# Optimization experiments

Hardware: AMD Instinct MI355X
Metric: run time of the kernel (lower is better)

## Reference

```python
import jax, jax.numpy as jnp
import numpy as np

H, W, NUM_HEADS = 32, 32, 8


def dwconv3x3(x, w, b):
    # x: (B,C,H,W), w: (C,1,3,3) depthwise, b: (C,)
    y = jax.lax.conv_general_dilated(
        x, w, window_strides=(1, 1), padding='SAME',
        dimension_numbers=('NCHW', 'OIHW', 'NCHW'),
        feature_group_count=x.shape[1])
    return y + b[None, :, None, None]


def conv1x1(x, w, b):
    # x: (B,C,H,W), w: (O,C), b: (O,)
    return jnp.einsum('oc,bchw->bohw', w, x) + b[None, :, None, None]


def layernorm(x, w, b, eps=1e-6):
    mu = x.mean(-1, keepdims=True)
    var = ((x - mu) ** 2).mean(-1, keepdims=True)
    return (x - mu) / jnp.sqrt(var + eps) * w + b


def setup_inputs() -> dict:
    key = jax.random.key(0)
    ks = jax.random.split(key, 12)
    B, N, C = 32, H * W, 512
    Ch = 4 * C  # inverted MLP hidden
    s_lin = 0.02
    s_dw = np.sqrt(2.0 / 9.0)   # fan_out init for 3x3 depthwise
    s_pw1 = np.sqrt(2.0 / Ch)
    s_pw2 = np.sqrt(2.0 / C)
    return {
        'x': jax.random.normal(ks[0], (B, N, C), jnp.float32),
        'cpe_w': jax.random.normal(ks[1], (C, 1, 3, 3), jnp.float32) * s_dw,
        'cpe_b': jnp.zeros((C,), jnp.float32),
        'ln1_w': jnp.ones((C,), jnp.float32),
        'ln1_b': jnp.zeros((C,), jnp.float32),
        'qkv_w': jax.random.normal(ks[2], (3 * C, C), jnp.float32) * s_lin,
        'crpe_w': jax.random.normal(ks[3], (C, 1, 3, 3), jnp.float32) * s_dw,
        'crpe_b': jnp.zeros((C,), jnp.float32),
        'ln2_w': jnp.ones((C,), jnp.float32),
        'ln2_b': jnp.zeros((C,), jnp.float32),
        'fc1_w': jax.random.normal(ks[4], (Ch, C), jnp.float32) * s_pw1,
        'fc1_b': jnp.zeros((Ch,), jnp.float32),
        'dw_w': jax.random.normal(ks[5], (Ch, 1, 3, 3), jnp.float32) * s_dw,
        'dw_b': jnp.zeros((Ch,), jnp.float32),
        'fc2_w': jax.random.normal(ks[6], (C, Ch), jnp.float32) * s_pw2,
        'fc2_b': jnp.zeros((C,), jnp.float32),
    }


def reference(x, cpe_w, cpe_b, ln1_w, ln1_b, qkv_w, crpe_w, crpe_b,
              ln2_w, ln2_b, fc1_w, fc1_b, dw_w, dw_b, fc2_w, fc2_b):
    B, N, C = x.shape
    h = NUM_HEADS
    d = C // h
    scale = d ** -0.5

    # --- Convolutional position encoding: x = x + dwconv(x) ---
    img = x.reshape(B, H, W, C).transpose(0, 3, 1, 2)  # B C H W
    img = img + dwconv3x3(img, cpe_w, cpe_b)
    x = img.transpose(0, 2, 3, 1).reshape(B, N, C)

    # --- Factorized attention + conv relative position encoding ---
    cur = layernorm(x, ln1_w, ln1_b)
    qkv = cur @ qkv_w.T                                 # (B,N,3C)
    qkv = qkv.reshape(B, N, 3, h, d).transpose(2, 0, 3, 1, 4)  # (3,B,h,N,d)
    q, k, v = qkv[0], qkv[1], qkv[2]
    k_softmax = jax.nn.softmax(k, axis=2)               # softmax over tokens N
    ktv = jnp.einsum('bhnk,bhnv->bhkv', k_softmax, v)   # (B,h,d,d)
    factor_att = jnp.einsum('bhnk,bhkv->bhnv', q, ktv)  # (B,h,N,d)
    # crpe: depthwise conv on v as image, elementwise-multiplied by q
    v_img = v.transpose(0, 1, 3, 2).reshape(B, h * d, H, W)
    v_img = dwconv3x3(v_img, crpe_w, crpe_b)
    v_conv = v_img.reshape(B, h, d, N).transpose(0, 1, 3, 2)
    crpe = q * v_conv
    attn_out = (scale * factor_att + crpe).transpose(0, 2, 1, 3).reshape(B, N, C)
    x = x + attn_out

    # --- Inverted MLP (conv-based channel mixing) ---
    cur = layernorm(x, ln2_w, ln2_b)
    img = cur.reshape(B, H, W, C).transpose(0, 3, 1, 2)  # B C H W
    hdn = conv1x1(img, fc1_w, fc1_b)
    hdn = jax.nn.gelu(hdn, approximate=False)
    hdn = hdn + dwconv3x3(hdn, dw_w, dw_b)
    out = conv1x1(hdn, fc2_w, fc2_b)
    x = x + out.transpose(0, 2, 3, 1).reshape(B, N, C)
    return x
```

## Files before the change

kernel.cpp:

```cpp
#include <hip/hip_runtime.h>
#include <hip/hip_bf16.h>

using bf16 = __hip_bfloat16;
using s16x4 = __attribute__((ext_vector_type(4))) short;
using s16x8 = __attribute__((ext_vector_type(8))) short;
using f32x4 = __attribute__((ext_vector_type(4))) float;

#define DI __device__ __forceinline__

template <int N> DI void wvm() {
    if constexpr (N == 8) asm volatile("s_waitcnt vmcnt(8)" ::: "memory");
    else if constexpr (N == 4) asm volatile("s_waitcnt vmcnt(4)" ::: "memory");
    else if constexpr (N == 2) asm volatile("s_waitcnt vmcnt(2)" ::: "memory");
    else asm volatile("s_waitcnt vmcnt(0)" ::: "memory");
}

DI float b2f(short s) { union { unsigned u; float f; } z; z.u = ((unsigned)(unsigned short)s) << 16; return z.f; }
DI short f2b(float f) { bf16 t = __float2bfloat16(f); return *(short*)&t; }

DI float gelu_f(float x) {
    const float t = 0.7978845608f * x * (1.f + 0.044715f * x * x);
    const float e = __expf(2.f * t);
    const float th = 1.f - 2.f / (e + 1.f);
    return 0.5f * x * (1.f + th);
}

DI void ld8(const bf16* p, float* f) {
    s16x8 x = *(const s16x8*)(const void*)p;
#pragma unroll
    for (int c = 0; c < 8; c++) f[c] = b2f(x[c]);
}
DI void ld8(const float* p, float* f) {
    float4 a = *(const float4*)p, b = *(const float4*)(p + 4);
    f[0]=a.x; f[1]=a.y; f[2]=a.z; f[3]=a.w; f[4]=b.x; f[5]=b.y; f[6]=b.z; f[7]=b.w;
}

typedef const __attribute__((address_space(1))) void* gp_t;
typedef __attribute__((address_space(3))) void* lp_t;
DI void gload_lds16(const void* g, void* l) {
    __builtin_amdgcn_global_load_lds((gp_t)g, (lp_t)l, 16, 0, 0);
}

__global__ void diag_k(float* out, float v) { out[0] = v; }

__global__ void f2bf_k(const float* __restrict__ in, bf16* __restrict__ out, int n) {
    int i = (blockIdx.x * 256 + threadIdx.x) * 8;
    if (i >= n) return;
    float f[8];
    ld8(in + i, f);
    s16x8 o;
#pragma unroll
    for (int c = 0; c < 8; c++) o[c] = f2b(f[c]);
    *(s16x8*)(void*)(out + i) = o;
}

__global__ void f2bf_w2_k(const float* __restrict__ in, bf16* __restrict__ out) {
    const int i = (blockIdx.x * 256 + threadIdx.x) * 8;
    const int n = i >> 11, c = i & 2047;
    const int h = c >> 10, k = c & 1023;
    float f[8];
    ld8(in + i, f);
    s16x8 o;
#pragma unroll
    for (int e = 0; e < 8; e++) o[e] = f2b(f[e]);
    *(s16x8*)(void*)(out + (size_t)h * 524288 + n * 1024 + k) = o;
}

DI void tap10(const float* r, float w0, float w1, float w2, float* acc) {
#pragma unroll
    for (int i = 0; i < 8; i++)
        acc[i] += w0 * r[i] + w1 * r[i + 1] + w2 * r[i + 2];
}

template <typename TI, typename TO, bool RESID, int CPL>
__global__ __launch_bounds__(256) void conv4_k(
    const TI* in, long rs, long coff,
    const float* __restrict__ w, const float* __restrict__ bias,
    TO* out, long ors, int gshift)
{
    constexpr int CH = 64 * CPL;
    constexpr int ECNT = CH / 8;
    __shared__ float buf[2][CH][33];
    const int t = threadIdx.x;
    const int band = blockIdx.x & 3;
    const int cg = (blockIdx.x >> 2) & ((1 << gshift) - 1);
    const int img = blockIdx.x >> (2 + gshift);
    const int y0 = band * 8;

    const int spx = t >> 3;
    const int sce = (t & 7) * ECNT;
    const TI* gsrc = in + ((long)img << 10) * rs + coff + (long)cg * CH + sce;

    const int c = t & 63;
    const int xb = (t >> 6) * 8;

    float wv9[9][CPL], bw[CPL];
#pragma unroll
    for (int p = 0; p < CPL; p++) {
        const int gch = cg * CH + c * CPL + p;
#pragma unroll
        for (int j = 0; j < 9; j++) wv9[j][p] = w[gch * 9 + j];
        bw[p] = bias[gch];
    }

    auto stage = [&](int row) {
        float f[ECNT];
        ld8(gsrc + (long)(row * 32 + spx) * rs, f);
        if constexpr (ECNT == 16) ld8(gsrc + (long)(row * 32 + spx) * rs + 8, f + 8);
        float* d = &buf[row & 1][0][0];
#pragma unroll
        for (int k = 0; k < ECNT; k++) {
            const int ch = sce + k;
            const int rr = (CPL == 2) ? ((ch & 1) * 64 + (ch >> 1)) : ch;
            d[rr * 33 + spx] = f[k];
        }
    };
    auto slice = [&](int row, float r[CPL][10]) {
#pragma unroll
        for (int p = 0; p < CPL; p++) {
            const float* s = &buf[row & 1][c + p * 64][0];
            r[p][0] = (xb == 0) ? 0.f : s[xb - 1];
#pragma unroll
            for (int i = 0; i < 8; i++) r[p][1 + i] = s[xb + i];
            r[p][9] = (xb + 8 >= 32) ? 0.f : s[xb + 8];
        }
    };
    auto zero = [&](float r[CPL][10]) {
#pragma unroll
        for (int p = 0; p < CPL; p++)
#pragma unroll
            for (int i = 0; i < 10; i++) r[p][i] = 0.f;
    };

    float r0[CPL][10], r1[CPL][10], r2[CPL][10];
    if (y0 > 0) stage(y0 - 1);
    __syncthreads();
    if (y0 > 0) slice(y0 - 1, r0); else zero(r0);
    stage(y0);
    __syncthreads();
    slice(y0, r1);

    for (int y = y0; y < y0 + 8; ++y) {
        const int yn = y + 1;
        if (yn <= 31) stage(yn);
        __syncthreads();
        if (yn <= 31) slice(yn, r2); else zero(r2);
        float acc[CPL][8];
#pragma unroll
        for (int p = 0; p < CPL; p++) {
#pragma unroll
            for (int i = 0; i < 8; i++) acc[p][i] = bw[p];
            tap10(r0[p], wv9[0][p], wv9[1][p], wv9[2][p], acc[p]);
            tap10(r1[p], wv9[3][p], wv9[4][p], wv9[5][p], acc[p]);
            tap10(r2[p], wv9[6][p], wv9[7][p], wv9[8][p], acc[p]);
            if (RESID) {
#pragma unroll
                for (int i = 0; i < 8; i++) acc[p][i] += r1[p][i + 1];
            }
        }
        TO* o = out + ((long)(img * 1024 + y * 32 + xb)) * ors + (long)cg * CH + c * CPL;
#pragma unroll
        for (int i = 0; i < 8; i++) {
            if constexpr (CPL == 2 && sizeof(TO) == 2) {
                const unsigned u = (unsigned)(unsigned short)f2b(acc[0][i]) |
                                   ((unsigned)(unsigned short)f2b(acc[1][i]) << 16);
                *(unsigned*)(void*)(o + (long)i * ors) = u;
            } else {
                o[(long)i * ors] = (TO)acc[0][i];
            }
        }
#pragma unroll
        for (int p = 0; p < CPL; p++)
#pragma unroll
            for (int i = 0; i < 10; i++) { r0[p][i] = r1[p][i]; r1[p][i] = r2[p][i]; }
    }
}

__global__ __launch_bounds__(256) void ln_k(const float* __restrict__ x,
                                            const float* __restrict__ w,
                                            const float* __restrict__ bp,
                                            bf16* __restrict__ out)
{
    const size_t row = blockIdx.x * 4 + (threadIdx.x >> 6);
    const int t = threadIdx.x & 63;
    const float* xr = x + row * 512;
    alignas(16) float v[8];
    *(float4*)&v[0] = *(const float4*)(xr + t * 8);
    *(float4*)&v[4] = *(const float4*)(xr + t * 8 + 4);
    float s = 0.f;
#pragma unroll
    for (int j = 0; j < 8; j++) s += v[j];
#pragma unroll
    for (int mm = 32; mm; mm >>= 1) s += __shfl_xor(s, mm);
    const float mu = s * (1.f / 512.f);
    float q = 0.f;
#pragma unroll
    for (int j = 0; j < 8; j++) { v[j] -= mu; q += v[j] * v[j]; }
#pragma unroll
    for (int mm = 32; mm; mm >>= 1) q += __shfl_xor(q, mm);
    const float rstd = rsqrtf(q * (1.f / 512.f) + 1e-6f);
    alignas(16) float wv[8], bv[8];
    *(float4*)&wv[0] = *(const float4*)(w + t * 8);
    *(float4*)&wv[4] = *(const float4*)(w + t * 8 + 4);
    *(float4*)&bv[0] = *(const float4*)(bp + t * 8);
    *(float4*)&bv[4] = *(const float4*)(bp + t * 8 + 4);
    alignas(16) bf16 o[8];
#pragma unroll
    for (int j = 0; j < 8; j++) o[j] = __float2bfloat16(v[j] * rstd * wv[j] + bv[j]);
    *(uint4*)(out + row * 512 + t * 8) = *(const uint4*)o;
}

template <int EPI, int K>
__global__ __launch_bounds__(512) void gemm8p_k(
    const bf16* __restrict__ A, const bf16* __restrict__ Bw,
    const float* __restrict__ bias, const float* resid,
    bf16* __restrict__ outb, float* outf, int M, int Nn)
{
    constexpr int KT = K / 64;
    __shared__ __align__(16) char lds[131072];
    char* ldsA = lds;
    char* ldsB = lds + 65536;
    const int t = threadIdx.x;
    const int lane = t & 63;
    const int w = t >> 6;
    const int wr = w >> 2, wc = w & 3;
    const int m0 = blockIdx.x * 256;
    const int n0 = blockIdx.y * 256;
    const int lr = lane & 15, lg = lane >> 4;

    f32x4 acc[8][4] = {};

    const int srow = lane >> 3;
    const int ssrc = 8 * ((lane & 7) ^ srow);

    auto SA = [&](int b, int kt, int h) {
#pragma unroll
        for (int j = 0; j < 2; j++) {
            const int lrow0 = j * 64 + w * 8;
            const int R0 = j * 128 + h * 64 + (lrow0 & 63);
            gload_lds16(A + (size_t)(m0 + R0 + srow) * K + kt * 64 + ssrc,
                        ldsA + ((b * 2 + h) * 128 + lrow0) * 128);
        }
    };
    auto SB = [&](int b, int kt, int h) {
#pragma unroll
        for (int j = 0; j < 2; j++) {
            const int lrow0 = j * 64 + w * 8;
            const int R0 = (lrow0 >> 5) * 64 + h * 32 + (lrow0 & 31);
            gload_lds16(Bw + (size_t)(n0 + R0 + srow) * K + kt * 64 + ssrc,
                        ldsB + ((b * 2 + h) * 128 + lrow0) * 128);
        }
    };
    auto RA = [&](int b, int h, int m, int ks) -> s16x8 {
        return *(const s16x8*)(ldsA + ((b * 2 + h) * 128 + wr * 64 + m * 16 + lr) * 128
                               + (((ks * 4 + lg) ^ (lr & 7)) << 4));
    };
    auto RB = [&](int b, int h, int n, int ks) -> s16x8 {
        return *(const s16x8*)(ldsB + ((b * 2 + h) * 128 + wc * 32 + n * 16 + lr) * 128
                               + (((ks * 4 + lg) ^ (lr & 7)) << 4));
    };
    auto MM = [&](int mb, int nb, s16x8 (&a)[2][4], s16x8 (&b)[2][2]) {
#pragma unroll
        for (int ks = 0; ks < 2; ks++)
#pragma unroll
            for (int m = 0; m < 4; m++)
#pragma unroll
                for (int n = 0; n < 2; n++)
                    acc[mb + m][nb + n] =
                        __builtin_amdgcn_mfma_f32_16x16x32_bf16(a[ks][m], b[ks][n], acc[mb + m][nb + n], 0, 0, 0);
    };

    SA(0, 0, 0); SB(0, 0, 0); SA(0, 0, 1); SB(0, 0, 1);
    SA(1, 1, 0); SB(1, 1, 0);
    wvm<8>();
    __builtin_amdgcn_s_barrier();

    s16x8 aLo[2][4], aHi[2][4], bLo[2][2], bHi[2][2];
    auto TILE = [&](int kt) {
        const int b = kt & 1;
#pragma unroll
        for (int ks = 0; ks < 2; ks++) {
#pragma unroll
            for (int m = 0; m < 4; m++) aLo[ks][m] = RA(b, 0, m, ks);
#pragma unroll
            for (int n = 0; n < 2; n++) bLo[ks][n] = RB(b, 0, n, ks);
        }
        if (kt + 1 < KT) SA(b ^ 1, kt + 1, 1);
        __builtin_amdgcn_s_barrier();
        __builtin_amdgcn_s_setprio(1);
        MM(0, 0, aLo, bLo);
        __builtin_amdgcn_s_setprio(0);
        if (kt + 1 < KT) wvm<8>(); else wvm<2>();
        __builtin_amdgcn_s_barrier();
#pragma unroll
        for (int ks = 0; ks < 2; ks++)
#pragma unroll
            for (int m = 0; m < 4; m++) aHi[ks][m] = RA(b, 1, m, ks);
        if (kt + 1 < KT) SB(b ^ 1, kt + 1, 1);
        __builtin_amdgcn_s_barrier();
        __builtin_amdgcn_s_setprio(1);
        MM(4, 0, aHi, bLo);
        __builtin_amdgcn_s_setprio(0);
        if (kt + 1 < KT) wvm<8>(); else wvm<0>();
        __builtin_amdgcn_s_barrier();
#pragma unroll
        for (int ks = 0; ks < 2; ks++)
#pragma unroll
            for (int n = 0; n < 2; n++) bHi[ks][n] = RB(b, 1, n, ks);
        if (kt + 2 < KT) SA(b, kt + 2, 0);
        __builtin_amdgcn_s_barrier();
        __builtin_amdgcn_s_setprio(1);
        MM(4, 2, aHi, bHi);
        __builtin_amdgcn_s_setprio(0);
        __builtin_amdgcn_s_barrier();
        if (kt + 2 < KT) SB(b, kt + 2, 0);
        __builtin_amdgcn_s_barrier();
        __builtin_amdgcn_s_setprio(1);
        MM(0, 2, aLo, bHi);
        __builtin_amdgcn_s_setprio(0);
        if (kt + 2 < KT) { wvm<8>(); __builtin_amdgcn_s_barrier(); }
        else if (kt + 1 < KT) { wvm<4>(); __builtin_amdgcn_s_barrier(); }
    };

    if constexpr (KT <= 8) {
#pragma unroll
        for (int kt = 0; kt < KT; ++kt) TILE(kt);
    } else {
#pragma unroll 2
        for (int kt = 0; kt < KT; ++kt) TILE(kt);
    }

#pragma unroll
    for (int i = 0; i < 8; i++) {
#pragma unroll
        for (int j = 0; j < 4; j++) {
            const int col = n0 + wc * 64 + j * 16 + lr;
            float bcol = 0.f;
            if constexpr (EPI == 1 || EPI == 2) bcol = bias[col];
#pragma unroll
            for (int r = 0; r < 4; r++) {
                const int row = m0 + wr * 128 + i * 16 + lg * 4 + r;
                float v = acc[i][j][r] + bcol;
                const size_t idx = (size_t)row * Nn + col;
                if (EPI >= 2) outf[idx] = v + resid[idx];
                else outb[idx] = __float2bfloat16(EPI == 1 ? gelu_f(v) : v);
            }
        }
    }
}

__global__ __launch_bounds__(256) void ktv_part_k(const bf16* __restrict__ qkv,
                                                  float* __restrict__ ktvp,
                                                  float* __restrict__ csp)
{
    const int b = blockIdx.x >> 5;
    const int hh = (blockIdx.x >> 2) & 7;
    const int sp = blockIdx.x & 3;
    const bf16* kb = qkv + (size_t)b * 1024 * 1536 + 512 + hh * 64;
    const bf16* vb = kb + 512;
    __shared__ __align__(16) bf16 Ks[16 * 64];
    __shared__ __align__(16) bf16 Vs[16 * 64];
    const int t = threadIdx.x;
    const int kk = t & 63, vg = t >> 6;
    float acc[16] = {};
    float psum = 0.f;
    const int sr = t >> 4, sc = (t & 15) * 4;
    for (int n0 = sp * 256; n0 < sp * 256 + 256; n0 += 16) {
        __syncthreads();
        *(s16x4*)(void*)(Ks + sr * 64 + sc) = *(const s16x4*)(const void*)(kb + (size_t)(n0 + sr) * 1536 + sc);
        *(s16x4*)(void*)(Vs + sr * 64 + sc) = *(const s16x4*)(const void*)(vb + (size_t)(n0 + sr) * 1536 + sc);
        __syncthreads();
#pragma unroll
        for (int i = 0; i < 16; i++) {
            const float p = __expf(b2f(*(const short*)(const void*)(Ks + i * 64 + kk)));
            psum += p;
            float vv[16];
            ld8(Vs + i * 64 + vg * 16, vv);
            ld8(Vs + i * 64 + vg * 16 + 8, vv + 8);
#pragma unroll
            for (int j = 0; j < 16; j++) acc[j] += p * vv[j];
        }
    }
    const int bh4 = (b * 8 + hh) * 4 + sp;
    float* o = ktvp + (size_t)bh4 * 4096 + kk * 64 + vg * 16;
#pragma unroll
    for (int j = 0; j < 16; j++) o[j] = acc[j];
    if (vg == 0) csp[bh4 * 64 + kk] = psum;
}

__global__ __launch_bounds__(256) void ktv_red_k(const float* __restrict__ ktvp,
                                                 const float* __restrict__ csp,
                                                 bf16* __restrict__ ktvT)
{
    const int bh = blockIdx.x;
    const int t = threadIdx.x;
#pragma unroll
    for (int i = 0; i < 16; i++) {
        const int e = t + 256 * i;
        const int kk = e >> 6, v = e & 63;
        float cs = 0.f, val = 0.f;
#pragma unroll
        for (int sp = 0; sp < 4; sp++) {
            cs += csp[(bh * 4 + sp) * 64 + kk];
            val += ktvp[(size_t)(bh * 4 + sp) * 4096 + e];
        }
        ktvT[(size_t)bh * 4096 + v * 64 + kk] = __float2bfloat16(val * (0.125f / cs));
    }
}

__global__ __launch_bounds__(256) void attnout2_k(
    float* xs, const bf16* __restrict__ qkv,
    const bf16* __restrict__ ktvT, const bf16* __restrict__ vc)
{
    __shared__ __align__(16) char qs[256 * 128];
    __shared__ __align__(16) char ks[64 * 128];
    const int t = threadIdx.x;
    const int bid = blockIdx.x;
    const int b = bid >> 5, hh = (bid >> 2) & 7, nc = bid & 3;
    const int n0 = nc * 256;
    const int lane = t & 63, w = t >> 6;
    const int lr = lane & 15, lg = lane >> 4;

    {
        const int r0 = t >> 3, sl = t & 7;
#pragma unroll
        for (int it = 0; it < 8; it++) {
            const int row = it * 32 + r0;
            const uint4 v = *(const uint4*)(qkv + ((size_t)(b * 1024 + n0 + row)) * 1536 + hh * 64 + sl * 8);
            *(uint4*)(qs + row * 128 + ((sl ^ (row & 7)) << 4)) = v;
        }
#pragma unroll
        for (int it = 0; it < 2; it++) {
            const int u = it * 256 + t;
            const int vr = u >> 3, sl2 = u & 7;
            const uint4 vv = *(const uint4*)(ktvT + (size_t)(b * 8 + hh) * 4096 + vr * 64 + sl2 * 8);
            *(uint4*)(ks + vr * 128 + ((sl2 ^ (vr & 7)) << 4)) = vv;
        }
    }
    __syncthreads();

    f32x4 acc[4][4] = {};
    s16x8 aF[2][4], bF[2][4];
#pragma unroll
    for (int ksi = 0; ksi < 2; ksi++) {
#pragma unroll
        for (int m = 0; m < 4; m++) {
            const int row = w * 64 + m * 16 + lr;
            aF[ksi][m] = *(const s16x8*)(qs + row * 128 + (((ksi * 4 + lg) ^ (lr & 7)) << 4));
        }
#pragma unroll
        for (int j = 0; j < 4; j++) {
            const int vr = j * 16 + lr;
            bF[ksi][j] = *(const s16x8*)(ks + vr * 128 + (((ksi * 4 + lg) ^ (lr & 7)) << 4));
        }
    }
#pragma unroll
    for (int ksi = 0; ksi < 2; ksi++)
#pragma unroll
        for (int m = 0; m < 4; m++)
#pragma unroll
            for (int j = 0; j < 4; j++)
                acc[m][j] = __builtin_amdgcn_mfma_f32_16x16x32_bf16(aF[ksi][m], bF[ksi][j], acc[m][j], 0, 0, 0);

#pragma unroll
    for (int m = 0; m < 4; m++) {
#pragma unroll
        for (int j = 0; j < 4; j++) {
#pragma unroll
            for (int r = 0; r < 4; r++) {
                const int lrow = w * 64 + m * 16 + lg * 4 + r;
                const int col = j * 16 + lr;
                const size_t idx = ((size_t)(b * 1024 + n0 + lrow)) * 512 + hh * 64 + col;
                const short qv = *(const short*)(qs + lrow * 128 + ((((col >> 3) ^ (lrow & 7)) << 4)) + (col & 7) * 2);
                xs[idx] = xs[idx] + acc[m][j][r] + b2f(qv) * __bfloat162float(vc[idx]);
            }
        }
    }
}

static constexpr size_t OFF_WQ   = 0;
static constexpr size_t OFF_W1   = 1572864;
static constexpr size_t OFF_W2   = 3670016;
static constexpr size_t OFF_CUR  = 5767168;
static constexpr size_t OFF_QKV  = 39321600;
static constexpr size_t OFF_VC   = 139984896;
static constexpr size_t OFF_KTVP = 173539328;
static constexpr size_t OFF_CSP  = 190316544;
static constexpr size_t OFF_KTV  = 190578688;
static constexpr size_t WS_NEED  = 194772992;
static constexpr size_t OFF_HG   = OFF_QKV;
static constexpr size_t OFF_H2   = OFF_QKV + 67108864;

extern "C" void kernel_launch(void* const* d_in, const int* in_sizes, int n_in,
                              void* d_out, int out_size, void* d_ws, size_t ws_size,
                              hipStream_t stream)
{
    const float* x     = (const float*)d_in[0];
    const float* cpe_w = (const float*)d_in[1];
    const float* cpe_b = (const float*)d_in[2];
    const float* ln1_w = (const float*)d_in[3];
    const float* ln1_b = (const float*)d_in[4];
    const float* qkv_w = (const float*)d_in[5];
    const float* crpe_w= (const float*)d_in[6];
    const float* crpe_b= (const float*)d_in[7];
    const float* ln2_w = (const float*)d_in[8];
    const float* ln2_b = (const float*)d_in[9];
    const float* fc1_w = (const float*)d_in[10];
    const float* fc1_b = (const float*)d_in[11];
    const float* dw_w  = (const float*)d_in[12];
    const float* dw_b  = (const float*)d_in[13];
    const float* fc2_w = (const float*)d_in[14];
    const float* fc2_b = (const float*)d_in[15];
    float* spine = (float*)d_out;
    char* ws = (char*)d_ws;

    if (ws_size < WS_NEED) {
        diag_k<<<1, 1, 0, stream>>>(spine, (float)ws_size);
        return;
    }

    bf16*  wq   = (bf16*)(ws + OFF_WQ);
    bf16*  w1   = (bf16*)(ws + OFF_W1);
    bf16*  w2r  = (bf16*)(ws + OFF_W2);
    bf16*  cur  = (bf16*)(ws + OFF_CUR);
    bf16*  qkv  = (bf16*)(ws + OFF_QKV);
    bf16*  vc   = (bf16*)(ws + OFF_VC);
    float* ktvp = (float*)(ws + OFF_KTVP);
    float* csp  = (float*)(ws + OFF_CSP);
    bf16*  ktvT = (bf16*)(ws + OFF_KTV);
    bf16*  hg   = (bf16*)(ws + OFF_HG);
    bf16*  h2   = (bf16*)(ws + OFF_H2);

    f2bf_k<<<(1536 * 512 / 8 + 255) / 256, 256, 0, stream>>>(qkv_w, wq, 1536 * 512);
    f2bf_k<<<(2048 * 512 / 8 + 255) / 256, 256, 0, stream>>>(fc1_w, w1, 2048 * 512);
    f2bf_w2_k<<<512 * 2048 / 8 / 256, 256, 0, stream>>>(fc2_w, w2r);

    conv4_k<float, float, true, 1><<<32 * 8 * 4, 256, 0, stream>>>(x, 512, 0, cpe_w, cpe_b, spine, 512, 3);

    const int M = 32768;
    ln_k<<<M / 4, 256, 0, stream>>>(spine, ln1_w, ln1_b, cur);
    gemm8p_k<0, 512><<<dim3(128, 6), 512, 0, stream>>>(cur, wq, nullptr, nullptr, qkv, nullptr, M, 1536);
    ktv_part_k<<<32 * 8 * 4, 256, 0, stream>>>(qkv, ktvp, csp);
    ktv_red_k<<<32 * 8, 256, 0, stream>>>(ktvp, csp, ktvT);
    conv4_k<bf16, bf16, false, 2><<<32 * 4 * 4, 256, 0, stream>>>(qkv, 1536, 1024, crpe_w, crpe_b, vc, 512, 2);
    attnout2_k<<<32 * 8 * 4, 256, 0, stream>>>(spine, qkv, ktvT, vc);
    ln_k<<<M / 4, 256, 0, stream>>>(spine, ln2_w, ln2_b, cur);

    for (int h = 0; h < 2; h++) {
        gemm8p_k<1, 512><<<dim3(128, 4), 512, 0, stream>>>(
            cur, w1 + (size_t)h * 1024 * 512, fc1_b + h * 1024, nullptr, hg, nullptr, M, 1024);
        conv4_k<bf16, bf16, true, 2><<<32 * 8 * 4, 256, 0, stream>>>(
            hg, 1024, 0, dw_w + (size_t)h * 1024 * 9, dw_b + h * 1024, h2, 1024, 3);
        if (h == 0)
            gemm8p_k<2, 1024><<<dim3(128, 2), 512, 0, stream>>>(
                h2, w2r, fc2_b, spine, nullptr, spine, M, 512);
        else
            gemm8p_k<3, 1024><<<dim3(128, 2), 512, 0, stream>>>(
                h2, w2r + (size_t)1 * 524288, nullptr, spine, nullptr, spine, M, 512);
    }
}
```

Baseline: 563.7 us.

## Compute K-softmax^T V with MFMA in a single fused kernel

Replaces the scalar FMA split-N partial kernel and its separate reduction kernel with one kernel per (batch, head). It stages exp(K) and V transposed into swizzled LDS and accumulates ktv with bf16 MFMA, computing column sums and normalization in-kernel. This removes one launch and the fp32 partial round-trip through global memory. In exchange, exp(K) is rounded to bf16 before the matmul, and the grid drops to 256 blocks iterating over all 1024 tokens serially.

```diff
diff --git a/kernel.cpp b/kernel.cpp
--- a/kernel.cpp
+++ b/kernel.cpp
@@ -349,62 +349,87 @@
     }
 }
 
-__global__ __launch_bounds__(256) void ktv_part_k(const bf16* __restrict__ qkv,
-                                                  float* __restrict__ ktvp,
-                                                  float* __restrict__ csp)
+__global__ __launch_bounds__(256) void ktv2_k(const bf16* __restrict__ qkv,
+                                              bf16* __restrict__ ktvT)
 {
-    const int b = blockIdx.x >> 5;
-    const int hh = (blockIdx.x >> 2) & 7;
-    const int sp = blockIdx.x & 3;
-    const bf16* kb = qkv + (size_t)b * 1024 * 1536 + 512 + hh * 64;
-    const bf16* vb = kb + 512;
-    __shared__ __align__(16) bf16 Ks[16 * 64];
-    __shared__ __align__(16) bf16 Vs[16 * 64];
+    __shared__ __align__(16) char P[64 * 128];
+    __shared__ __align__(16) char Vt[64 * 128];
+    __shared__ float csl[64 * 5];
     const int t = threadIdx.x;
-    const int kk = t & 63, vg = t >> 6;
-    float acc[16] = {};
-    float psum = 0.f;
-    const int sr = t >> 4, sc = (t & 15) * 4;
-    for (int n0 = sp * 256; n0 < sp * 256 + 256; n0 += 16) {
+    const int b = blockIdx.x >> 3, hh = blockIdx.x & 7;
+    const int lane = t & 63, w = t >> 6;
+    const int lr = lane & 15, lg = lane >> 4;
+
+    const int n_r = t >> 2;
+    const int k0 = (t & 3) * 16;
+    const bf16* kbase = qkv + (size_t)(b * 1024) * 1536 + 512 + hh * 64 + k0;
+    const bf16* vbase = kbase + 512;
+
+    const int kq = t & 63, qq = t >> 6;
+    float cacc = 0.f;
+
+    f32x4 acc[4] = {};
+
+    for (int n0 = 0; n0 < 1024; n0 += 64) {
+        const uint4 ka = *(const uint4*)(kbase + (size_t)(n0 + n_r) * 1536);
+        const uint4 kb2 = *(const uint4*)(kbase + (size_t)(n0 + n_r) * 1536 + 8);
+        const uint4 va = *(const uint4*)(vbase + (size_t)(n0 + n_r) * 1536);
+        const uint4 vb2 = *(const uint4*)(vbase + (size_t)(n0 + n_r) * 1536 + 8);
         __syncthreads();
-        *(s16x4*)(void*)(Ks + sr * 64 + sc) = *(const s16x4*)(const void*)(kb + (size_t)(n0 + sr) * 1536 + sc);
-        *(s16x4*)(void*)(Vs + sr * 64 + sc) = *(const s16x4*)(const void*)(vb + (size_t)(n0 + sr) * 1536 + sc);
+        {
+            const short* ke = (const short*)&ka;
+            const short* ke2 = (const short*)&kb2;
+            const short* ve = (const short*)&va;
+            const short* ve2 = (const short*)&vb2;
+            const int nslot = ((n_r >> 3) << 4);
+            const int nbyte = (n_r & 7) * 2;
+#pragma unroll
+            for (int j = 0; j < 16; j++) {
+                const int row = k0 + j;
+                const short kv = j < 8 ? ke[j] : ke2[j - 8];
+                const short vv = j < 8 ? ve[j] : ve2[j - 8];
+                const int off = row * 128 + (nslot ^ ((row & 7) << 4)) + nbyte;
+                *(short*)(P + off) = f2b(__expf(b2f(kv)));
+                *(short*)(Vt + off) = vv;
+            }
+        }
         __syncthreads();
-#pragma unroll
-        for (int i = 0; i < 16; i++) {
-            const float p = __expf(b2f(*(const short*)(const void*)(Ks + i * 64 + kk)));
-            psum += p;
-            float vv[16];
-            ld8(Vs + i * 64 + vg * 16, vv);
-            ld8(Vs + i * 64 + vg * 16 + 8, vv + 8);
-#pragma unroll
-            for (int j = 0; j < 16; j++) acc[j] += p * vv[j];
-        }
-    }
-    const int bh4 = (b * 8 + hh) * 4 + sp;
-    float* o = ktvp + (size_t)bh4 * 4096 + kk * 64 + vg * 16;
-#pragma unroll
-    for (int j = 0; j < 16; j++) o[j] = acc[j];
-    if (vg == 0) csp[bh4 * 64 + kk] = psum;
-}
-
-__global__ __launch_bounds__(256) void ktv_red_k(const float* __restrict__ ktvp,
-                                                 const float* __restrict__ csp,
-                                                 bf16* __restrict__ ktvT)
-{
-    const int bh = blockIdx.x;
-    const int t = threadIdx.x;
-#pragma unroll
-    for (int i = 0; i < 16; i++) {
-        const int e = t + 256 * i;
-        const int kk = e >> 6, v = e & 63;
-        float cs = 0.f, val = 0.f;
-#pragma unroll
-        for (int sp = 0; sp < 4; sp++) {
-            cs += csp[(bh * 4 + sp) * 64 + kk];
-            val += ktvp[(size_t)(bh * 4 + sp) * 4096 + e];
-        }
-        ktvT[(size_t)bh * 4096 + v * 64 + kk] = __float2bfloat16(val * (0.125f / cs));
+        {
+            const char* pr = P + kq * 128;
+            const int sw = (kq & 7) << 4;
+            s16x8 x0 = *(const s16x8*)(pr + (((qq * 2) << 4) ^ sw));
+            s16x8 x1 = *(const s16x8*)(pr + (((qq * 2 + 1) << 4) ^ sw));
+#pragma unroll
+            for (int j = 0; j < 8; j++) cacc += b2f(x0[j]) + b2f(x1[j]);
+        }
+#pragma unroll
+        for (int ks2 = 0; ks2 < 2; ks2++) {
+            s16x8 aF = *(const s16x8*)(Vt + (w * 16 + lr) * 128 + (((ks2 * 4 + lg) ^ (lr & 7)) << 4));
+            s16x8 bF[4];
+#pragma unroll
+            for (int j = 0; j < 4; j++)
+                bF[j] = *(const s16x8*)(P + (j * 16 + lr) * 128 + (((ks2 * 4 + lg) ^ (lr & 7)) << 4));
+#pragma unroll
+            for (int j = 0; j < 4; j++)
+                acc[j] = __builtin_amdgcn_mfma_f32_16x16x32_bf16(aF, bF[j], acc[j], 0, 0, 0);
+        }
+    }
+    __syncthreads();
+    csl[kq * 5 + qq] = cacc;
+    __syncthreads();
+    if (t < 64) csl[t * 5 + 4] = csl[t * 5] + csl[t * 5 + 1] + csl[t * 5 + 2] + csl[t * 5 + 3];
+    __syncthreads();
+
+    bf16* o = ktvT + (size_t)(b * 8 + hh) * 4096;
+#pragma unroll
+    for (int j = 0; j < 4; j++) {
+        const int col = j * 16 + lr;
+        const float sc = 0.125f / csl[col * 5 + 4];
+#pragma unroll
+        for (int r = 0; r < 4; r++) {
+            const int vrow = w * 16 + lg * 4 + r;
+            o[vrow * 64 + col] = __float2bfloat16(acc[j][r] * sc);
+        }
     }
 }
 
@@ -484,9 +509,7 @@
 static constexpr size_t OFF_CUR  = 5767168;
 static constexpr size_t OFF_QKV  = 39321600;
 static constexpr size_t OFF_VC   = 139984896;
-static constexpr size_t OFF_KTVP = 173539328;
-static constexpr size_t OFF_CSP  = 190316544;
-static constexpr size_t OFF_KTV  = 190578688;
+static constexpr size_t OFF_KTV  = 173539328;
 static constexpr size_t WS_NEED  = 194772992;
 static constexpr size_t OFF_HG   = OFF_QKV;
 static constexpr size_t OFF_H2   = OFF_QKV + 67108864;
@@ -525,8 +548,6 @@
     bf16*  cur  = (bf16*)(ws + OFF_CUR);
     bf16*  qkv  = (bf16*)(ws + OFF_QKV);
     bf16*  vc   = (bf16*)(ws + OFF_VC);
-    float* ktvp = (float*)(ws + OFF_KTVP);
-    float* csp  = (float*)(ws + OFF_CSP);
     bf16*  ktvT = (bf16*)(ws + OFF_KTV);
     bf16*  hg   = (bf16*)(ws + OFF_HG);
     bf16*  h2   = (bf16*)(ws + OFF_H2);
@@ -540,8 +561,7 @@
     const int M = 32768;
     ln_k<<<M / 4, 256, 0, stream>>>(spine, ln1_w, ln1_b, cur);
     gemm8p_k<0, 512><<<dim3(128, 6), 512, 0, stream>>>(cur, wq, nullptr, nullptr, qkv, nullptr, M, 1536);
-    ktv_part_k<<<32 * 8 * 4, 256, 0, stream>>>(qkv, ktvp, csp);
-    ktv_red_k<<<32 * 8, 256, 0, stream>>>(ktvp, csp, ktvT);
+    ktv2_k<<<256, 256, 0, stream>>>(qkv, ktvT);
     conv4_k<bf16, bf16, false, 2><<<32 * 4 * 4, 256, 0, stream>>>(qkv, 1536, 1024, crpe_w, crpe_b, vc, 512, 2);
     attnout2_k<<<32 * 8 * 4, 256, 0, stream>>>(spine, qkv, ktvT, vc);
     ln_k<<<M / 4, 256, 0, stream>>>(spine, ln2_w, ln2_b, cur);
```

Result: faster. 510.4 us (-9.5%).
